# Kernel tuning notes

Measured on AMD Instinct MI355X. Metric: run time of the kernel, lower is better.

## Reference

```python
import jax, jax.numpy as jnp
import numpy as np

B = 1
T, H, W = 8, 20, 20
N = T * H * W  # 3200
DIM = 3072
NH = 24
HD = DIM // NH  # 128
D_T, D_H, D_W = 32, 48, 48  # 3D RoPE split of head_dim
EPS = 1e-6


def _axis_freqs(d, n):
    # [n, d//2] angles for one axis
    inv = 1.0 / (10000.0 ** (jnp.arange(0, d, 2, dtype=jnp.float32) / d))
    return jnp.arange(n, dtype=jnp.float32)[:, None] * inv[None, :]


def rope3d_cos_sin(t, h, w):
    ft = jnp.broadcast_to(_axis_freqs(D_T, t)[:, None, None, :], (t, h, w, D_T // 2))
    fh = jnp.broadcast_to(_axis_freqs(D_H, h)[None, :, None, :], (t, h, w, D_H // 2))
    fw = jnp.broadcast_to(_axis_freqs(D_W, w)[None, None, :, :], (t, h, w, D_W // 2))
    f = jnp.concatenate([ft, fh, fw], axis=-1).reshape(t * h * w, HD // 2)
    return jnp.cos(f), jnp.sin(f)


def apply_rope(x, cos, sin):
    # x: [B, N, NH, HD]; interleaved pairs rotation
    xf = x.astype(jnp.float32).reshape(*x.shape[:-1], HD // 2, 2)
    x1, x2 = xf[..., 0], xf[..., 1]
    c = cos[None, :, None, :]
    s = sin[None, :, None, :]
    r1 = x1 * c - x2 * s
    r2 = x1 * s + x2 * c
    return jnp.stack([r1, r2], axis=-1).reshape(x.shape).astype(x.dtype)


def rmsnorm(x, w):
    xf = x.astype(jnp.float32)
    n = xf * jax.lax.rsqrt(jnp.mean(xf * xf, axis=-1, keepdims=True) + EPS)
    return (n * w).astype(x.dtype)


def setup_inputs() -> dict:
    key = jax.random.key(0)
    ks = jax.random.split(key, 6)
    scale = 0.02
    return {
        "x": jax.random.normal(ks[0], (B, N, DIM), jnp.float32),
        "Wq": jax.random.normal(ks[1], (DIM, DIM), jnp.float32) * scale,
        "bq": jnp.zeros((DIM,), jnp.float32),
        "Wk": jax.random.normal(ks[2], (DIM, DIM), jnp.float32) * scale,
        "bk": jnp.zeros((DIM,), jnp.float32),
        "Wv": jax.random.normal(ks[3], (DIM, DIM), jnp.float32) * scale,
        "bv": jnp.zeros((DIM,), jnp.float32),
        "Wo": jax.random.normal(ks[4], (DIM, DIM), jnp.float32) * scale,
        "bo": jnp.zeros((DIM,), jnp.float32),
        "q_norm_w": jnp.ones((HD,), jnp.float32),
        "k_norm_w": jnp.ones((HD,), jnp.float32),
        "num_cond_latents": 2,
    }


def reference(x, Wq, bq, Wk, bk, Wv, bv, Wo, bo, q_norm_w, k_norm_w, num_cond_latents):
    # QKV projections -> [B, N, NH, HD]
    q = (x @ Wq + bq).reshape(B, N, NH, HD)
    k = (x @ Wk + bk).reshape(B, N, NH, HD)
    v = (x @ Wv + bv).reshape(B, N, NH, HD)
    # per-head RMSNorm on q, k
    q = rmsnorm(q, q_norm_w)
    k = rmsnorm(k, k_norm_w)
    # 3D RoPE over (T, H, W) grid
    cos, sin = rope3d_cos_sin(T, H, W)
    q = apply_rope(q, cos, sin)
    k = apply_rope(k, cos, sin)
    # I2V split: cond tokens attend only to themselves; noise tokens attend to all
    nct = num_cond_latents * (N // T)  # static python int
    out_cond = jax.nn.dot_product_attention(q[:, :nct], k[:, :nct], v[:, :nct])
    out_noise = jax.nn.dot_product_attention(q[:, nct:], k, v)
    out = jnp.concatenate([out_cond, out_noise], axis=1).reshape(B, N, DIM)
    return out @ Wo + bo
```

## Files before the change

kernel.cpp:

```cpp
#include <hip/hip_runtime.h>
#include <stdint.h>

typedef _Float16 f16;
typedef _Float16 f16x2 __attribute__((ext_vector_type(2)));
typedef _Float16 f16x4 __attribute__((ext_vector_type(4)));
typedef _Float16 f16x8 __attribute__((ext_vector_type(8)));
typedef float f32x4 __attribute__((ext_vector_type(4)));
typedef float f32x16 __attribute__((ext_vector_type(16)));

#define DIM   3072
#define NTOK  3200
#define NHEAD 24
#define SCALE 0.08838834764831845f

__device__ __forceinline__ void async16(const void* g, void* l) {
  __builtin_amdgcn_global_load_lds(
      (const __attribute__((address_space(1))) uint32_t*)g,
      (__attribute__((address_space(3))) uint32_t*)l, 16, 0, 0);
}

__device__ __forceinline__ uint32_t pkrtz(float a, float b) {
  auto p = __builtin_amdgcn_cvt_pkrtz(a, b);
  return __builtin_bit_cast(uint32_t, p);
}


__global__ __launch_bounds__(256) void cvt_f32_f16(const float* __restrict__ in,
                                                   f16* __restrict__ out) {
  size_t i = ((size_t)blockIdx.x * 256 + threadIdx.x) * 4;
  float4 v = *(const float4*)(in + i);
  f16x4 o = {(f16)v.x, (f16)v.y, (f16)v.z, (f16)v.w};
  *(f16x4*)(out + i) = o;
}

__global__ __launch_bounds__(256) void transpose4(
    const float* __restrict__ W0, const float* __restrict__ W1,
    const float* __restrict__ W2, const float* __restrict__ W3,
    f16* __restrict__ T0, f16* __restrict__ T1,
    f16* __restrict__ T2, f16* __restrict__ T3) {
  const float* W; f16* T;
  switch (blockIdx.z) {
    case 0: W = W0; T = T0; break;
    case 1: W = W1; T = T1; break;
    case 2: W = W2; T = T2; break;
    default: W = W3; T = T3; break;
  }
  __shared__ float t[32][33];
  int tx = threadIdx.x & 31, ty = threadIdx.x >> 5;
  size_t bx = (size_t)blockIdx.x * 32, by = (size_t)blockIdx.y * 32;
#pragma unroll
  for (int r = 0; r < 4; ++r)
    t[ty + r * 8][tx] = W[(by + ty + r * 8) * DIM + bx + tx];
  __syncthreads();
#pragma unroll
  for (int r = 0; r < 4; ++r)
    T[(bx + ty + r * 8) * DIM + by + tx] = (f16)t[tx][ty + r * 8];
}

__global__ __launch_bounds__(256) void rope_tables(float* __restrict__ cosT,
                                                   float* __restrict__ sinT) {
  int tid = blockIdx.x * 256 + threadIdx.x;
  int p = tid >> 6, j = tid & 63;
  int t = p / 400, rem = p % 400;
  int hh = rem / 20, ww = rem % 20;
  float val, e;
  if (j < 16)      { val = (float)t;  e = (float)(2 * j)        * (1.f / 32.f); }
  else if (j < 40) { val = (float)hh; e = (float)(2 * (j - 16)) * (1.f / 48.f); }
  else             { val = (float)ww; e = (float)(2 * (j - 40)) * (1.f / 48.f); }
  float f = val * expf(-e * 9.210340371976184f);
  cosT[tid] = cosf(f);
  sinT[tid] = sinf(f);
}


__device__ __forceinline__ void gemm_body(const f16* __restrict__ A,
                                          const f16* __restrict__ B,
                                          const float* __restrict__ bias,
                                          void* __restrict__ C, int m0, int n0,
                                          int mode) {
  __shared__ f16 As[128 * 32];
  __shared__ f16 Bs[128 * 32];
  const int tid = threadIdx.x;
  const int lane = tid & 63, w = tid >> 6;
  const int l15 = lane & 15, l4 = lane >> 4;
  const int wr = (w >> 1) * 64, wc = (w & 1) * 64;
  f32x4 acc[4][4];
#pragma unroll
  for (int m = 0; m < 4; ++m)
#pragma unroll
    for (int n = 0; n < 4; ++n) acc[m][n] = (f32x4){0.f, 0.f, 0.f, 0.f};

  for (int k0 = 0; k0 < DIM; k0 += 32) {
    __syncthreads();
#pragma unroll
    for (int c = 0; c < 2; ++c) {
      int bi = (w * 2 + c) * 1024 + lane * 16;
      int row = bi >> 6, off = bi & 63;
      async16((const char*)(A + (size_t)(m0 + row) * DIM + k0) + off,
              (char*)As + (w * 2 + c) * 1024);
      async16((const char*)(B + (size_t)(n0 + row) * DIM + k0) + off,
              (char*)Bs + (w * 2 + c) * 1024);
    }
    __syncthreads();
    f16x8 af[4], bf[4];
#pragma unroll
    for (int m = 0; m < 4; ++m)
      af[m] = *(const f16x8*)(As + (wr + m * 16 + l15) * 32 + l4 * 8);
#pragma unroll
    for (int n = 0; n < 4; ++n)
      bf[n] = *(const f16x8*)(Bs + (wc + n * 16 + l15) * 32 + l4 * 8);
#pragma unroll
    for (int m = 0; m < 4; ++m)
#pragma unroll
      for (int n = 0; n < 4; ++n)
        acc[m][n] = __builtin_amdgcn_mfma_f32_16x16x32_f16(af[m], bf[n], acc[m][n], 0, 0, 0);
  }
#pragma unroll
  for (int n = 0; n < 4; ++n) {
    int col = n0 + wc + n * 16 + l15;
    float bb = bias[col];
#pragma unroll
    for (int m = 0; m < 4; ++m) {
      int rbase = m0 + wr + m * 16 + l4 * 4;
      if (mode == 2) {
        f16x4 ov;
#pragma unroll
        for (int r = 0; r < 4; ++r) ov[r] = (f16)(acc[m][n][r] + bb);
        *(f16x4*)((f16*)C + (size_t)col * NTOK + rbase) = ov;
      } else if (mode == 1) {
#pragma unroll
        for (int r = 0; r < 4; ++r)
          ((float*)C)[(size_t)(rbase + r) * DIM + col] = acc[m][n][r] + bb;
      } else {
#pragma unroll
        for (int r = 0; r < 4; ++r)
          ((f16*)C)[(size_t)(rbase + r) * DIM + col] = (f16)(acc[m][n][r] + bb);
      }
    }
  }
}

__global__ __launch_bounds__(256) void gemm_qkv(
    const f16* __restrict__ A,
    const f16* __restrict__ B0, const f16* __restrict__ B1, const f16* __restrict__ B2,
    const float* __restrict__ b0, const float* __restrict__ b1, const float* __restrict__ b2,
    f16* __restrict__ C0, f16* __restrict__ C1, f16* __restrict__ C2) {
  int sel = blockIdx.y / 24, yn = blockIdx.y % 24;
  const f16* B = sel == 0 ? B0 : (sel == 1 ? B1 : B2);
  const float* bias = sel == 0 ? b0 : (sel == 1 ? b1 : b2);
  f16* C = sel == 0 ? C0 : (sel == 1 ? C1 : C2);
  gemm_body(A, B, bias, C, blockIdx.x * 128, yn * 128, sel == 2 ? 2 : 0);
}

__global__ __launch_bounds__(256) void gemm_out(
    const f16* __restrict__ A, const f16* __restrict__ B,
    const float* __restrict__ bias, float* __restrict__ C) {
  gemm_body(A, B, bias, C, blockIdx.x * 128, blockIdx.y * 128, 1);
}

__global__ __launch_bounds__(256) void rmsnorm_rope(
    f16* __restrict__ qk, const float* __restrict__ w,
    const float* __restrict__ cosT, const float* __restrict__ sinT, float osc) {
  int lane = threadIdx.x & 63, rb = threadIdx.x >> 6;
  int row = blockIdx.x * 4 + rb;
  int p = row / NHEAD;
  f16* ptr = qk + (size_t)row * 128 + lane * 2;
  f16x2 hv = *(const f16x2*)ptr;
  float x1 = (float)hv[0], x2 = (float)hv[1];
  float ss = x1 * x1 + x2 * x2;
#pragma unroll
  for (int o = 32; o > 0; o >>= 1) ss += __shfl_xor(ss, o);
  float r = rsqrtf(ss * (1.f / 128.f) + 1e-6f);
  float n1 = x1 * r * w[lane * 2], n2 = x2 * r * w[lane * 2 + 1];
  float c = cosT[p * 64 + lane], s = sinT[p * 64 + lane];
  f16x2 ov = {(f16)((n1 * c - n2 * s) * osc), (f16)((n1 * s + n2 * c) * osc)};
  *(f16x2*)ptr = ov;
}

__global__ __launch_bounds__(320) void attn2(
    const f16* __restrict__ q, const f16* __restrict__ k, const f16* __restrict__ vt,
    f16* __restrict__ out) {
  extern __shared__ char smem[];
  f16* Ks = (f16*)smem;
  f16* Vs = (f16*)(smem + 32768);

  int L = blockIdx.x;
  int c = L & 7, j = L >> 3;
  int head = c * 3 + j / 20, qblk = j % 20;
  int q0 = qblk * 160;
  int kv_len = (q0 < 800) ? 800 : 3200;

  const int tid = threadIdx.x, lane = tid & 63, w = tid >> 6;
  const int l31 = lane & 31, hi = lane >> 5;
  const int qg = q0 + w * 32 + l31;
  const int sw_base = l31 & 15;

  f16x8 qr[8];
#pragma unroll
  for (int ks = 0; ks < 8; ++ks)
    qr[ks] = *(const f16x8*)(q + (size_t)qg * DIM + head * 128 + ks * 16 + hi * 8);

  f32x16 o[4];
#pragma unroll
  for (int mb = 0; mb < 4; ++mb)
#pragma unroll
    for (int r = 0; r < 16; ++r) o[mb][r] = 0.f;
  float m_run = -1e30f, l_run = 0.f;

  for (int t0 = 0; t0 < kv_len; t0 += 128) {
    __syncthreads();
#pragma unroll
    for (int r = 0; r < 13; ++r) {
      int idx = r * 320 + tid;
      if (idx < 4096) {
        int row = (idx >> 4) & 127;
        int sw = (idx & 15) ^ (row & 15);
        const f16* src;
        if (idx < 2048) src = k + (size_t)(t0 + row) * DIM + head * 128 + sw * 8;
        else            src = vt + ((size_t)head * 128 + row) * NTOK + t0 + sw * 8;
        async16(src, (char*)(idx < 2048 ? Ks : Vs) + (idx & 2047) * 16);
      }
    }
    __syncthreads();

    const int nvb = min(4, (kv_len - t0) >> 5);

    f32x16 s4[4];
#pragma unroll
    for (int b = 0; b < 4; ++b)
#pragma unroll
      for (int r = 0; r < 16; ++r) s4[b][r] = 0.f;
#pragma unroll
    for (int ks = 0; ks < 8; ++ks) {
#pragma unroll
      for (int b = 0; b < 4; ++b) {
        if (b < nvb) {
          const f16x8 kf = *(const f16x8*)(Ks + ((b * 32 + l31) << 7) +
                                           (((ks * 2 + hi) ^ sw_base) << 3));
          s4[b] = __builtin_amdgcn_mfma_f32_32x32x16_f16(kf, qr[ks], s4[b], 0, 0, 0);
        }
      }
    }

    float tmax = -1e30f;
#pragma unroll
    for (int b = 0; b < 4; ++b)
      if (b < nvb)
#pragma unroll
        for (int r = 0; r < 16; ++r) tmax = fmaxf(tmax, s4[b][r]);
    tmax = fmaxf(tmax, __shfl_xor(tmax, 32));
    if (!__all(tmax <= m_run + 8.f)) {
      float mn = fmaxf(m_run, tmax);
      float alpha = __expf(m_run - mn);
      l_run *= alpha;
#pragma unroll
      for (int mb = 0; mb < 4; ++mb)
#pragma unroll
        for (int r = 0; r < 16; ++r) o[mb][r] *= alpha;
      m_run = mn;
    }
    float rs = 0.f;
#pragma unroll
    for (int b = 0; b < 4; ++b)
      if (b < nvb)
#pragma unroll
        for (int r = 0; r < 16; ++r) {
          float e = __expf(s4[b][r] - m_run);
          s4[b][r] = e;
          rs += e;
        }
    l_run += rs;

    const int nks = nvb * 2;
#pragma unroll
    for (int ks = 0; ks < 8; ++ks) {
      if (ks < nks) {
        const int b = ks >> 1, s8 = (ks & 1) * 8;
        uint32_t a0 = pkrtz(s4[b][s8 + 0], s4[b][s8 + 1]);
        uint32_t b0 = pkrtz(s4[b][s8 + 4], s4[b][s8 + 5]);
        asm("v_permlane32_swap_b32 %0, %1" : "+v"(a0), "+v"(b0));
        uint32_t a1 = pkrtz(s4[b][s8 + 2], s4[b][s8 + 3]);
        uint32_t b1 = pkrtz(s4[b][s8 + 6], s4[b][s8 + 7]);
        asm("v_permlane32_swap_b32 %0, %1" : "+v"(a1), "+v"(b1));
        union { uint32_t u[4]; f16x8 v; } pf;
        pf.u[0] = a0; pf.u[1] = a1; pf.u[2] = b0; pf.u[3] = b1;
#pragma unroll
        for (int mb = 0; mb < 4; ++mb) {
          const f16x8 vf = *(const f16x8*)(Vs + ((mb * 32 + l31) << 7) +
                                           (((ks * 2 + hi) ^ sw_base) << 3));
          o[mb] = __builtin_amdgcn_mfma_f32_32x32x16_f16(vf, pf.v, o[mb], 0, 0, 0);
        }
      }
    }
  }

  l_run += __shfl_xor(l_run, 32);
  float inv = 1.f / l_run;
#pragma unroll
  for (int mb = 0; mb < 4; ++mb)
#pragma unroll
    for (int jq = 0; jq < 4; ++jq) {
      f16x4 ov;
#pragma unroll
      for (int e = 0; e < 4; ++e) ov[e] = (f16)(o[mb][jq * 4 + e] * inv);
      *(f16x4*)(out + (size_t)qg * DIM + head * 128 + mb * 32 + jq * 8 + hi * 4) = ov;
    }
}


extern "C" void kernel_launch(void* const* d_in, const int* in_sizes, int n_in,
                              void* d_out, int out_size, void* d_ws, size_t ws_size,
                              hipStream_t stream) {
  const float* x   = (const float*)d_in[0];
  const float* Wq  = (const float*)d_in[1];
  const float* bq  = (const float*)d_in[2];
  const float* Wk  = (const float*)d_in[3];
  const float* bk  = (const float*)d_in[4];
  const float* Wv  = (const float*)d_in[5];
  const float* bv  = (const float*)d_in[6];
  const float* Wo  = (const float*)d_in[7];
  const float* bo  = (const float*)d_in[8];
  const float* qnw = (const float*)d_in[9];
  const float* knw = (const float*)d_in[10];

  char* ws = (char*)d_ws;
  f16*   xb   = (f16*)(ws);
  f16*   WqT  = (f16*)(ws + 19660800);
  f16*   WkT  = (f16*)(ws + 38535168);
  f16*   WvT  = (f16*)(ws + 57409536);
  f16*   WoT  = (f16*)(ws + 76283904);
  f16*   qb   = (f16*)(ws + 95158272);
  f16*   kb   = (f16*)(ws + 114819072);
  f16*   vtb  = (f16*)(ws + 134479872);
  f16*   ab   = (f16*)(ws + 154140672);
  float* cosT = (float*)(ws + 173801472);
  float* sinT = (float*)(ws + 174620672);

  cvt_f32_f16<<<9600, 256, 0, stream>>>(x, xb);
  transpose4<<<dim3(96, 96, 4), 256, 0, stream>>>(Wq, Wk, Wv, Wo, WqT, WkT, WvT, WoT);
  rope_tables<<<800, 256, 0, stream>>>(cosT, sinT);

  gemm_qkv<<<dim3(25, 72), 256, 0, stream>>>(xb, WqT, WkT, WvT, bq, bk, bv, qb, kb, vtb);

  rmsnorm_rope<<<19200, 256, 0, stream>>>(qb, qnw, cosT, sinT, SCALE);
  rmsnorm_rope<<<19200, 256, 0, stream>>>(kb, knw, cosT, sinT, 1.0f);

  attn2<<<480, 320, 65536, stream>>>(qb, kb, vtb, ab);

  gemm_out<<<dim3(25, 24), 256, 0, stream>>>(ab, WoT, bo, (float*)d_out);
}
```

Before: 651.9 us.

## Replace 128x128 GEMMs with pipelined 256x256 double-buffered swizzled MFMA GEMM

```diff
diff --git a/kernel.cpp b/kernel.cpp
--- a/kernel.cpp
+++ b/kernel.cpp
@@ -22,6 +22,10 @@
 __device__ __forceinline__ uint32_t pkrtz(float a, float b) {
   auto p = __builtin_amdgcn_cvt_pkrtz(a, b);
   return __builtin_bit_cast(uint32_t, p);
+}
+
+__device__ __forceinline__ f32x4 mfma16(f16x8 a, f16x8 b, f32x4 c) {
+  return __builtin_amdgcn_mfma_f32_16x16x32_f16(a, b, c, 0, 0, 0);
 }
 
 
@@ -73,89 +77,175 @@
 }
 
 
-__device__ __forceinline__ void gemm_body(const f16* __restrict__ A,
-                                          const f16* __restrict__ B,
-                                          const float* __restrict__ bias,
-                                          void* __restrict__ C, int m0, int n0,
-                                          int mode) {
-  __shared__ f16 As[128 * 32];
-  __shared__ f16 Bs[128 * 32];
+__device__ __forceinline__ void stage_half(const f16* __restrict__ base, int row0,
+                                           int rowmax, int k0, char* ldsdst, int tid) {
+#pragma unroll
+  for (int s = 0; s < 2; ++s) {
+    int idx = s * 512 + tid;
+    int r = idx >> 3, pc = idx & 7;
+    int cc = pc ^ (r & 7);
+    int grow = row0 + r;
+    grow = grow < rowmax ? grow : rowmax - 1;
+    async16(base + (size_t)grow * DIM + k0 + cc * 8, ldsdst + idx * 16);
+  }
+}
+
+__device__ __forceinline__ void gemm256_body(
+    const f16* __restrict__ A, const f16* __restrict__ Bm,
+    const float* __restrict__ bias, void* __restrict__ C,
+    int m0, int n0, int Mrows, int mode, char* smem) {
+
   const int tid = threadIdx.x;
   const int lane = tid & 63, w = tid >> 6;
+  const int wm = w >> 2, wn = w & 3;
   const int l15 = lane & 15, l4 = lane >> 4;
-  const int wr = (w >> 1) * 64, wc = (w & 1) * 64;
-  f32x4 acc[4][4];
-#pragma unroll
-  for (int m = 0; m < 4; ++m)
+
+  f32x4 acc[8][4];
+#pragma unroll
+  for (int m = 0; m < 8; ++m)
 #pragma unroll
     for (int n = 0; n < 4; ++n) acc[m][n] = (f32x4){0.f, 0.f, 0.f, 0.f};
 
-  for (int k0 = 0; k0 < DIM; k0 += 32) {
-    __syncthreads();
-#pragma unroll
-    for (int c = 0; c < 2; ++c) {
-      int bi = (w * 2 + c) * 1024 + lane * 16;
-      int row = bi >> 6, off = bi & 63;
-      async16((const char*)(A + (size_t)(m0 + row) * DIM + k0) + off,
-              (char*)As + (w * 2 + c) * 1024);
-      async16((const char*)(B + (size_t)(n0 + row) * DIM + k0) + off,
-              (char*)Bs + (w * 2 + c) * 1024);
-    }
-    __syncthreads();
-    f16x8 af[4], bf[4];
-#pragma unroll
-    for (int m = 0; m < 4; ++m)
-      af[m] = *(const f16x8*)(As + (wr + m * 16 + l15) * 32 + l4 * 8);
-#pragma unroll
-    for (int n = 0; n < 4; ++n)
-      bf[n] = *(const f16x8*)(Bs + (wc + n * 16 + l15) * 32 + l4 * 8);
-#pragma unroll
-    for (int m = 0; m < 4; ++m)
-#pragma unroll
-      for (int n = 0; n < 4; ++n)
-        acc[m][n] = __builtin_amdgcn_mfma_f32_16x16x32_f16(af[m], bf[n], acc[m][n], 0, 0, 0);
+  const int NT = DIM / 64;
+
+  stage_half(A,  m0,       Mrows,   0,  smem + 0,     tid);
+  stage_half(Bm, n0,       1 << 30, 0,  smem + 32768, tid);
+  stage_half(A,  m0 + 128, Mrows,   0,  smem + 16384, tid);
+  stage_half(Bm, n0 + 128, 1 << 30, 0,  smem + 49152, tid);
+  stage_half(A,  m0,       Mrows,   64, smem + 65536, tid);
+  asm volatile("s_waitcnt vmcnt(2)" ::: "memory");
+  __builtin_amdgcn_s_barrier();
+
+  const int arow0 = wm * 128 + l15;
+  const int brow0 = wn * 64 + l15;
+
+  for (int t = 0; t < NT; ++t) {
+    char* bufc = smem + (t & 1) * 65536;
+    char* bufn = smem + ((t + 1) & 1) * 65536;
+    const f16* Ald = (const f16*)bufc;
+    const f16* Bld = (const f16*)(bufc + 32768);
+    int k1 = (t + 1) * 64; k1 = k1 <= DIM - 64 ? k1 : DIM - 64;
+    int k2 = (t + 2) * 64; k2 = k2 <= DIM - 64 ? k2 : DIM - 64;
+
+    f16x8 af[8], b0, b1;
+
+#pragma unroll
+    for (int m = 0; m < 8; ++m) {
+      int r = arow0 + m * 16, pc = l4 ^ (r & 7);
+      af[m] = *(const f16x8*)(Ald + r * 64 + pc * 8);
+    }
+    { int r = brow0,      pc = l4 ^ (r & 7); b0 = *(const f16x8*)(Bld + r * 64 + pc * 8);
+      r = brow0 + 16;     pc = l4 ^ (r & 7); b1 = *(const f16x8*)(Bld + r * 64 + pc * 8); }
+    stage_half(Bm, n0, 1 << 30, k1, bufn + 32768, tid);
+    __builtin_amdgcn_s_barrier();
+    asm volatile("s_waitcnt lgkmcnt(0)" ::: "memory");
+    __builtin_amdgcn_sched_barrier(0);
+    __builtin_amdgcn_s_setprio(1);
+#pragma unroll
+    for (int m = 0; m < 8; ++m) {
+      acc[m][0] = mfma16(af[m], b0, acc[m][0]);
+      acc[m][1] = mfma16(af[m], b1, acc[m][1]);
+    }
+    __builtin_amdgcn_s_setprio(0);
+    __builtin_amdgcn_s_barrier();
+
+    { int r = brow0 + 32, pc = l4 ^ (r & 7); b0 = *(const f16x8*)(Bld + r * 64 + pc * 8);
+      r = brow0 + 48;     pc = l4 ^ (r & 7); b1 = *(const f16x8*)(Bld + r * 64 + pc * 8); }
+    stage_half(A, m0 + 128, Mrows, k1, bufn + 16384, tid);
+    __builtin_amdgcn_s_barrier();
+    asm volatile("s_waitcnt lgkmcnt(0)" ::: "memory");
+    __builtin_amdgcn_sched_barrier(0);
+    __builtin_amdgcn_s_setprio(1);
+#pragma unroll
+    for (int m = 0; m < 8; ++m) {
+      acc[m][2] = mfma16(af[m], b0, acc[m][2]);
+      acc[m][3] = mfma16(af[m], b1, acc[m][3]);
+    }
+    __builtin_amdgcn_s_setprio(0);
+    __builtin_amdgcn_s_barrier();
+
+#pragma unroll
+    for (int m = 0; m < 8; ++m) {
+      int r = arow0 + m * 16, pc = (4 + l4) ^ (r & 7);
+      af[m] = *(const f16x8*)(Ald + r * 64 + pc * 8);
+    }
+    { int r = brow0,      pc = (4 + l4) ^ (r & 7); b0 = *(const f16x8*)(Bld + r * 64 + pc * 8);
+      r = brow0 + 16;     pc = (4 + l4) ^ (r & 7); b1 = *(const f16x8*)(Bld + r * 64 + pc * 8); }
+    stage_half(Bm, n0 + 128, 1 << 30, k1, bufn + 49152, tid);
+    __builtin_amdgcn_s_barrier();
+    asm volatile("s_waitcnt lgkmcnt(0)" ::: "memory");
+    __builtin_amdgcn_sched_barrier(0);
+    __builtin_amdgcn_s_setprio(1);
+#pragma unroll
+    for (int m = 0; m < 8; ++m) {
+      acc[m][0] = mfma16(af[m], b0, acc[m][0]);
+      acc[m][1] = mfma16(af[m], b1, acc[m][1]);
+    }
+    __builtin_amdgcn_s_setprio(0);
+    __builtin_amdgcn_s_barrier();
+
+    { int r = brow0 + 32, pc = (4 + l4) ^ (r & 7); b0 = *(const f16x8*)(Bld + r * 64 + pc * 8);
+      r = brow0 + 48;     pc = (4 + l4) ^ (r & 7); b1 = *(const f16x8*)(Bld + r * 64 + pc * 8); }
+    stage_half(A, m0, Mrows, k2, bufc + 0, tid);
+    __builtin_amdgcn_s_barrier();
+    asm volatile("s_waitcnt lgkmcnt(0)" ::: "memory");
+    __builtin_amdgcn_sched_barrier(0);
+    __builtin_amdgcn_s_setprio(1);
+#pragma unroll
+    for (int m = 0; m < 8; ++m) {
+      acc[m][2] = mfma16(af[m], b0, acc[m][2]);
+      acc[m][3] = mfma16(af[m], b1, acc[m][3]);
+    }
+    __builtin_amdgcn_s_setprio(0);
+    asm volatile("s_waitcnt vmcnt(2)" ::: "memory");
+    __builtin_amdgcn_s_barrier();
   }
+
 #pragma unroll
   for (int n = 0; n < 4; ++n) {
-    int col = n0 + wc + n * 16 + l15;
+    int col = n0 + wn * 64 + n * 16 + l15;
     float bb = bias[col];
 #pragma unroll
-    for (int m = 0; m < 4; ++m) {
-      int rbase = m0 + wr + m * 16 + l4 * 4;
-      if (mode == 2) {
-        f16x4 ov;
-#pragma unroll
-        for (int r = 0; r < 4; ++r) ov[r] = (f16)(acc[m][n][r] + bb);
-        *(f16x4*)((f16*)C + (size_t)col * NTOK + rbase) = ov;
-      } else if (mode == 1) {
-#pragma unroll
-        for (int r = 0; r < 4; ++r)
-          ((float*)C)[(size_t)(rbase + r) * DIM + col] = acc[m][n][r] + bb;
-      } else {
-#pragma unroll
-        for (int r = 0; r < 4; ++r)
-          ((f16*)C)[(size_t)(rbase + r) * DIM + col] = (f16)(acc[m][n][r] + bb);
+    for (int m = 0; m < 8; ++m) {
+      int rbase = m0 + wm * 128 + m * 16 + l4 * 4;
+      if (rbase < Mrows) {
+        if (mode == 2) {
+          f16x4 ov;
+#pragma unroll
+          for (int r = 0; r < 4; ++r) ov[r] = (f16)(acc[m][n][r] + bb);
+          *(f16x4*)((f16*)C + (size_t)col * NTOK + rbase) = ov;
+        } else if (mode == 1) {
+#pragma unroll
+          for (int r = 0; r < 4; ++r)
+            ((float*)C)[(size_t)(rbase + r) * DIM + col] = acc[m][n][r] + bb;
+        } else {
+#pragma unroll
+          for (int r = 0; r < 4; ++r)
+            ((f16*)C)[(size_t)(rbase + r) * DIM + col] = (f16)(acc[m][n][r] + bb);
+        }
       }
     }
   }
 }
 
-__global__ __launch_bounds__(256) void gemm_qkv(
+__global__ __launch_bounds__(512, 2) void gemm256_qkv(
     const f16* __restrict__ A,
     const f16* __restrict__ B0, const f16* __restrict__ B1, const f16* __restrict__ B2,
     const float* __restrict__ b0, const float* __restrict__ b1, const float* __restrict__ b2,
     f16* __restrict__ C0, f16* __restrict__ C1, f16* __restrict__ C2) {
-  int sel = blockIdx.y / 24, yn = blockIdx.y % 24;
+  __shared__ char smem[131072];
+  int sel = blockIdx.y / 12, yn = blockIdx.y % 12;
   const f16* B = sel == 0 ? B0 : (sel == 1 ? B1 : B2);
   const float* bias = sel == 0 ? b0 : (sel == 1 ? b1 : b2);
   f16* C = sel == 0 ? C0 : (sel == 1 ? C1 : C2);
-  gemm_body(A, B, bias, C, blockIdx.x * 128, yn * 128, sel == 2 ? 2 : 0);
-}
-
-__global__ __launch_bounds__(256) void gemm_out(
+  gemm256_body(A, B, bias, C, blockIdx.x * 256, yn * 256, NTOK, sel == 2 ? 2 : 0, smem);
+}
+
+__global__ __launch_bounds__(512, 2) void gemm256_out(
     const f16* __restrict__ A, const f16* __restrict__ B,
     const float* __restrict__ bias, float* __restrict__ C) {
-  gemm_body(A, B, bias, C, blockIdx.x * 128, blockIdx.y * 128, 1);
+  __shared__ char smem[131072];
+  gemm256_body(A, B, bias, C, blockIdx.x * 256, blockIdx.y * 256, NTOK, 1, smem);
 }
 
 __global__ __launch_bounds__(256) void rmsnorm_rope(
@@ -340,12 +430,12 @@
   transpose4<<<dim3(96, 96, 4), 256, 0, stream>>>(Wq, Wk, Wv, Wo, WqT, WkT, WvT, WoT);
   rope_tables<<<800, 256, 0, stream>>>(cosT, sinT);
 
-  gemm_qkv<<<dim3(25, 72), 256, 0, stream>>>(xb, WqT, WkT, WvT, bq, bk, bv, qb, kb, vtb);
+  gemm256_qkv<<<dim3(13, 36), 512, 0, stream>>>(xb, WqT, WkT, WvT, bq, bk, bv, qb, kb, vtb);
 
   rmsnorm_rope<<<19200, 256, 0, stream>>>(qb, qnw, cosT, sinT, SCALE);
   rmsnorm_rope<<<19200, 256, 0, stream>>>(kb, knw, cosT, sinT, 1.0f);
 
   attn2<<<480, 320, 65536, stream>>>(qb, kb, vtb, ab);
 
-  gemm_out<<<dim3(25, 24), 256, 0, stream>>>(ab, WoT, bo, (float*)d_out);
-}
+  gemm256_out<<<dim3(13, 12), 512, 0, stream>>>(ab, WoT, bo, (float*)d_out);
+}
```

New measurement: 559.1 us. 14.2% less time.
